# Kernel tuning notes

Hardware: AMD Instinct MI355X
Metric: run time of the kernel (lower is better)

The kernel has to match this reference:

```python
import jax, jax.numpy as jnp
import numpy as np

N, OUT, IN = 16384, 2048, 2048

def setup_inputs() -> dict:
    key = jax.random.key(0)
    k1, k2, k3 = jax.random.split(key, 3)
    input_ = jax.random.normal(k1, (N, IN), dtype=jnp.float32)
    # kaiming normal, fan_in mode: std = sqrt(2/fan_in)
    weight = jax.random.normal(k2, (OUT, IN), dtype=jnp.float32) * np.sqrt(2.0 / IN)
    mask = jax.random.randint(k3, (OUT, IN), 0, 2, dtype=jnp.int32)
    return {"input_": input_, "weight": weight, "mask": mask}

def reference(input_, weight, mask):
    # out = x @ (W * mask)^T  -- mask is a fixed binary expander pattern
    masked_w = weight * mask.astype(weight.dtype)  # [OUT, IN]
    return jnp.matmul(input_, masked_w.T)          # [N, OUT]
```

## Files before the change

### kernel.cpp

```cpp
#include <hip/hip_runtime.h>


#define MDIM 16384
#define NDIM 2048
#define KDIM 2048

#define BM 256
#define BN 256
#define GRID_X ((MDIM / BM) * (NDIM / BN))

using f32x4   = __attribute__((ext_vector_type(4))) float;
using bf16x8  = __attribute__((ext_vector_type(8))) __bf16;
using ushort8 = __attribute__((ext_vector_type(8))) unsigned short;

typedef __attribute__((address_space(3))) const unsigned short* lds_cptr_t;

__device__ __forceinline__ unsigned short f2bf(float f) {
  unsigned int u = __builtin_bit_cast(unsigned int, f);
  u = u + 0x7FFFu + ((u >> 16) & 1u);
  return (unsigned short)(u >> 16);
}


__global__ void convert_input_kernel(const float* __restrict__ in,
                                     unsigned short* __restrict__ out) {
  size_t base = ((size_t)blockIdx.x * blockDim.x + threadIdx.x) * 8;
  float4 a = *reinterpret_cast<const float4*>(in + base);
  float4 b = *reinterpret_cast<const float4*>(in + base + 4);
  ushort8 v;
  v[0] = f2bf(a.x); v[1] = f2bf(a.y); v[2] = f2bf(a.z); v[3] = f2bf(a.w);
  v[4] = f2bf(b.x); v[5] = f2bf(b.y); v[6] = f2bf(b.z); v[7] = f2bf(b.w);
  *reinterpret_cast<ushort8*>(out + base) = v;
}

__global__ void convert_weight_kernel(const float* __restrict__ w,
                                      const int* __restrict__ mk,
                                      unsigned short* __restrict__ out) {
  size_t base = ((size_t)blockIdx.x * blockDim.x + threadIdx.x) * 8;
  float4 a = *reinterpret_cast<const float4*>(w + base);
  float4 b = *reinterpret_cast<const float4*>(w + base + 4);
  int4 m0 = *reinterpret_cast<const int4*>(mk + base);
  int4 m1 = *reinterpret_cast<const int4*>(mk + base + 4);
  ushort8 v;
  v[0] = m0.x ? f2bf(a.x) : (unsigned short)0;
  v[1] = m0.y ? f2bf(a.y) : (unsigned short)0;
  v[2] = m0.z ? f2bf(a.z) : (unsigned short)0;
  v[3] = m0.w ? f2bf(a.w) : (unsigned short)0;
  v[4] = m1.x ? f2bf(b.x) : (unsigned short)0;
  v[5] = m1.y ? f2bf(b.y) : (unsigned short)0;
  v[6] = m1.z ? f2bf(b.z) : (unsigned short)0;
  v[7] = m1.w ? f2bf(b.w) : (unsigned short)0;
  *reinterpret_cast<ushort8*>(out + base) = v;
}


__device__ __forceinline__ f32x4 MF(bf16x8 a, bf16x8 b, f32x4 c) {
  return __builtin_amdgcn_mfma_f32_16x16x32_bf16(a, b, c, 0, 0, 0);
}
#define VMCNT(n) asm volatile("s_waitcnt vmcnt(" #n ")" ::: "memory")
#define DSR(dst, p, off)                                                        \
  asm volatile("ds_read_b128 %0, %1 offset:%2" : "=v"(dst) : "v"(p), "i"(off))

__global__ __launch_bounds__(512, 2) void gemm_asm(
    const unsigned short* __restrict__ Abf,
    const unsigned short* __restrict__ Bbf,
    float* __restrict__ C) {
  __shared__ __attribute__((aligned(16))) unsigned short Asl[4 * 8192];
  __shared__ __attribute__((aligned(16))) unsigned short Bsl[4 * 8192];

  int bid = blockIdx.x;
  int wgs = (bid & 7) * (GRID_X / 8) + (bid >> 3);
  int tm = wgs >> 3;
  int tn = wgs & 7;
  int row0 = tm * BM, col0 = tn * BN;

  int t = threadIdx.x;
  int lane = t & 63, wid = t >> 6;
  int wr = wid >> 2, wc = wid & 3;
  int fr = lane & 15, fq = lane >> 4;

  int p0 = (wid * 2) * 64 + lane;
  int r0 = p0 >> 2, kc0 = ((p0 & 3) ^ ((r0 >> 1) & 3)) * 8;
  size_t offA0 = (size_t)(row0 + r0) * KDIM + kc0;
  size_t offB0 = (size_t)(col0 + r0) * KDIM + kc0;
  int ldsw0 = (wid * 2) * 512;

  int kxor = (fq ^ ((fr >> 1) & 3)) * 8;
  int aoff = (wr * 128 + fr) * 32 + kxor;
  int boff = (wc * 64 + fr) * 32 + kxor;
  lds_cptr_t aA = ((lds_cptr_t)Asl) + aoff;
  lds_cptr_t aB = ((lds_cptr_t)Bsl) + boff;

  f32x4 acc[8][4];
#pragma unroll
  for (int m = 0; m < 8; ++m)
#pragma unroll
    for (int n = 0; n < 4; ++n) acc[m][n] = f32x4{0.f, 0.f, 0.f, 0.f};

#define SLOT_A(b, kh) (Asl + ((b) * 2 + (kh)) * 8192)
#define SLOT_B(b, kh) (Bsl + ((b) * 2 + (kh)) * 8192)

#define STG(slot, base, o0, ke) do {                                            \
  __builtin_amdgcn_global_load_lds(                                             \
      (const __attribute__((address_space(1))) void*)((base) + (o0) + (ke)),    \
      (__attribute__((address_space(3))) void*)((slot) + ldsw0), 16, 0, 0);     \
  __builtin_amdgcn_global_load_lds(                                             \
      (const __attribute__((address_space(1))) void*)((base) + (o0) + 32768 +   \
                                                      (ke)),                    \
      (__attribute__((address_space(3))) void*)((slot) + ldsw0 + 512), 16, 0,   \
      0);                                                                       \
} while (0)

#define PHASE(b, kh, STAGES, WAITS) do {                                        \
  bf16x8 _afr[8], _bfr[4];                                                      \
  DSR(_afr[0], aA, ((b) * 2 + (kh)) * 16384 + 0 * 1024);                        \
  DSR(_afr[1], aA, ((b) * 2 + (kh)) * 16384 + 1 * 1024);                        \
  DSR(_afr[2], aA, ((b) * 2 + (kh)) * 16384 + 2 * 1024);                        \
  DSR(_afr[3], aA, ((b) * 2 + (kh)) * 16384 + 3 * 1024);                        \
  DSR(_afr[4], aA, ((b) * 2 + (kh)) * 16384 + 4 * 1024);                        \
  DSR(_afr[5], aA, ((b) * 2 + (kh)) * 16384 + 5 * 1024);                        \
  DSR(_afr[6], aA, ((b) * 2 + (kh)) * 16384 + 6 * 1024);                        \
  DSR(_afr[7], aA, ((b) * 2 + (kh)) * 16384 + 7 * 1024);                        \
  DSR(_bfr[0], aB, ((b) * 2 + (kh)) * 16384 + 0 * 1024);                        \
  DSR(_bfr[1], aB, ((b) * 2 + (kh)) * 16384 + 1 * 1024);                        \
  DSR(_bfr[2], aB, ((b) * 2 + (kh)) * 16384 + 2 * 1024);                        \
  DSR(_bfr[3], aB, ((b) * 2 + (kh)) * 16384 + 3 * 1024);                        \
  STAGES;                                                                       \
  WAITS;                                                                        \
  __builtin_amdgcn_s_barrier();                                                 \
  asm volatile("s_waitcnt lgkmcnt(0)" ::: "memory");                            \
  __builtin_amdgcn_sched_barrier(0);                                            \
  __builtin_amdgcn_s_setprio(1);                                                \
  _Pragma("unroll")                                                             \
  for (int _m = 0; _m < 8; ++_m)                                                \
    _Pragma("unroll")                                                           \
    for (int _n = 0; _n < 4; ++_n)                                              \
      acc[_m][_n] = MF(_afr[_m], _bfr[_n], acc[_m][_n]);                        \
  __builtin_amdgcn_s_setprio(0);                                                \
  __builtin_amdgcn_s_barrier();                                                 \
} while (0)

  STG(SLOT_A(0, 0), Abf, offA0, 0);
  STG(SLOT_B(0, 0), Bbf, offB0, 0);
  STG(SLOT_A(0, 1), Abf, offA0, 32);
  STG(SLOT_B(0, 1), Bbf, offB0, 32);
  STG(SLOT_A(1, 0), Abf, offA0, 64);
  STG(SLOT_B(1, 0), Bbf, offB0, 64);
  VMCNT(8);
  __builtin_amdgcn_s_barrier();

  for (int i = 0; i < 15; ++i) {
    int kb = i * 128;
    PHASE(0, 0, { STG(SLOT_A(1, 1), Abf, offA0, kb + 96);
                  STG(SLOT_B(1, 1), Bbf, offB0, kb + 96); }, VMCNT(8));
    PHASE(0, 1, { STG(SLOT_A(0, 0), Abf, offA0, kb + 128);
                  STG(SLOT_B(0, 0), Bbf, offB0, kb + 128); }, VMCNT(8));
    PHASE(1, 0, { STG(SLOT_A(0, 1), Abf, offA0, kb + 160);
                  STG(SLOT_B(0, 1), Bbf, offB0, kb + 160); }, VMCNT(8));
    PHASE(1, 1, { STG(SLOT_A(1, 0), Abf, offA0, kb + 192);
                  STG(SLOT_B(1, 0), Bbf, offB0, kb + 192); }, VMCNT(8));
  }
  {
    int kb = (15) * 128;
    PHASE(0, 0, { STG(SLOT_A(1, 1), Abf, offA0, kb + 96);
                  STG(SLOT_B(1, 1), Bbf, offB0, kb + 96); }, VMCNT(8));
    PHASE(0, 1, , VMCNT(4));
    PHASE(1, 0, , VMCNT(0));
    PHASE(1, 1, , );
  }

  size_t crow = (size_t)(row0 + wr * 128 + fq * 4);
  int ccol = col0 + wc * 64 + fr;
#pragma unroll
  for (int m = 0; m < 8; ++m)
#pragma unroll
    for (int n = 0; n < 4; ++n) {
      float* cp = C + (crow + m * 16) * NDIM + ccol + n * 16;
#pragma unroll
      for (int e = 0; e < 4; ++e) cp[(size_t)e * NDIM] = acc[m][n][e];
    }
#undef PHASE
#undef STG
#undef SLOT_A
#undef SLOT_B
}


__global__ __launch_bounds__(256) void gemm_fused_fallback(
    const float* __restrict__ Afp,
    const float* __restrict__ Wfp,
    const int* __restrict__ Mk,
    float* __restrict__ C) {
  __shared__ unsigned short As[128 * 32];
  __shared__ unsigned short Bs[128 * 32];
  int bid = blockIdx.x;
  int nwg = (MDIM / 128) * (NDIM / 128);
  int wg = (bid & 7) * (nwg / 8) + (bid >> 3);
  int tm = wg >> 4, tn = wg & 15;
  int row0 = tm * 128, col0 = tn * 128;
  int t = threadIdx.x;
  int lane = t & 63, wv = t >> 6;
  int wr = wv >> 1, wc = wv & 1;
  int fr = lane & 15, fq = lane >> 4;
  f32x4 acc[4][4];
#pragma unroll
  for (int i = 0; i < 4; ++i)
#pragma unroll
    for (int j = 0; j < 4; ++j) acc[i][j] = f32x4{0.f, 0.f, 0.f, 0.f};
  for (int kt = 0; kt < KDIM; kt += 32) {
#pragma unroll
    for (int j = 0; j < 2; ++j) {
      int c = j * 256 + t;
      int r = c >> 2;
      int ko = (c & 3) * 8;
      const float* ga = Afp + (size_t)(row0 + r) * KDIM + kt + ko;
      float4 a0 = *reinterpret_cast<const float4*>(ga);
      float4 a1 = *reinterpret_cast<const float4*>(ga + 4);
      ushort8 va;
      va[0] = f2bf(a0.x); va[1] = f2bf(a0.y); va[2] = f2bf(a0.z); va[3] = f2bf(a0.w);
      va[4] = f2bf(a1.x); va[5] = f2bf(a1.y); va[6] = f2bf(a1.z); va[7] = f2bf(a1.w);
      *reinterpret_cast<ushort8*>(As + (size_t)c * 8) = va;
      const float* gw = Wfp + (size_t)(col0 + r) * KDIM + kt + ko;
      const int* gm = Mk + (size_t)(col0 + r) * KDIM + kt + ko;
      float4 w0 = *reinterpret_cast<const float4*>(gw);
      float4 w1 = *reinterpret_cast<const float4*>(gw + 4);
      int4 m0 = *reinterpret_cast<const int4*>(gm);
      int4 m1 = *reinterpret_cast<const int4*>(gm + 4);
      ushort8 vb;
      vb[0] = m0.x ? f2bf(w0.x) : (unsigned short)0;
      vb[1] = m0.y ? f2bf(w0.y) : (unsigned short)0;
      vb[2] = m0.z ? f2bf(w0.z) : (unsigned short)0;
      vb[3] = m0.w ? f2bf(w0.w) : (unsigned short)0;
      vb[4] = m1.x ? f2bf(w1.x) : (unsigned short)0;
      vb[5] = m1.y ? f2bf(w1.y) : (unsigned short)0;
      vb[6] = m1.z ? f2bf(w1.z) : (unsigned short)0;
      vb[7] = m1.w ? f2bf(w1.w) : (unsigned short)0;
      *reinterpret_cast<ushort8*>(Bs + (size_t)c * 8) = vb;
    }
    __syncthreads();
    bf16x8 af[4], bfr[4];
#pragma unroll
    for (int m2 = 0; m2 < 4; ++m2)
      af[m2] = *reinterpret_cast<const bf16x8*>(As + (wr * 64 + m2 * 16 + fr) * 32 + fq * 8);
#pragma unroll
    for (int n2 = 0; n2 < 4; ++n2)
      bfr[n2] = *reinterpret_cast<const bf16x8*>(Bs + (wc * 64 + n2 * 16 + fr) * 32 + fq * 8);
#pragma unroll
    for (int m2 = 0; m2 < 4; ++m2)
#pragma unroll
      for (int n2 = 0; n2 < 4; ++n2)
        acc[m2][n2] = MF(af[m2], bfr[n2], acc[m2][n2]);
    __syncthreads();
  }
#pragma unroll
  for (int m2 = 0; m2 < 4; ++m2)
#pragma unroll
    for (int n2 = 0; n2 < 4; ++n2) {
      size_t r0 = (size_t)(row0 + wr * 64 + m2 * 16 + fq * 4);
      size_t c0 = (size_t)(col0 + wc * 64 + n2 * 16 + fr);
#pragma unroll
      for (int i = 0; i < 4; ++i) C[(r0 + i) * NDIM + c0] = acc[m2][n2][i];
    }
}


extern "C" void kernel_launch(void* const* d_in, const int* in_sizes, int n_in,
                              void* d_out, int out_size, void* d_ws, size_t ws_size,
                              hipStream_t stream) {
  const float* input  = (const float*)d_in[0];
  const float* weight = (const float*)d_in[1];
  const int*   mask   = (const int*)d_in[2];
  float* out = (float*)d_out;

  const size_t needA = (size_t)MDIM * KDIM * sizeof(unsigned short);
  const size_t needB = (size_t)NDIM * KDIM * sizeof(unsigned short);

  if (ws_size >= needA + needB) {
    unsigned short* Abf = (unsigned short*)d_ws;
    unsigned short* Bbf = (unsigned short*)((char*)d_ws + needA);
    convert_input_kernel<<<(MDIM * (size_t)KDIM / 8) / 256, 256, 0, stream>>>(input, Abf);
    convert_weight_kernel<<<(NDIM * (size_t)KDIM / 8) / 256, 256, 0, stream>>>(weight, mask, Bbf);
    gemm_asm<<<GRID_X, 512, 0, stream>>>(Abf, Bbf, out);
  } else {
    int nwg = (MDIM / 128) * (NDIM / 128);
    gemm_fused_fallback<<<nwg, 256, 0, stream>>>(input, weight, mask, out);
  }
}
```

Measured before the change: 174.6 us.

## Double-buffer LDS fragment reads in registers across GEMM phases

Measured after the change: 173.1 us. Within noise of the previous version (-0.9%).

```diff
diff --git a/kernel.cpp b/kernel.cpp
--- a/kernel.cpp
+++ b/kernel.cpp
@@ -61,7 +61,7 @@
 #define DSR(dst, p, off)                                                        \
   asm volatile("ds_read_b128 %0, %1 offset:%2" : "=v"(dst) : "v"(p), "i"(off))
 
-__global__ __launch_bounds__(512, 2) void gemm_asm(
+__global__ __launch_bounds__(512, 2) void gemm_ra(
     const unsigned short* __restrict__ Abf,
     const unsigned short* __restrict__ Bbf,
     float* __restrict__ C) {
@@ -96,6 +96,8 @@
   for (int m = 0; m < 8; ++m)
 #pragma unroll
     for (int n = 0; n < 4; ++n) acc[m][n] = f32x4{0.f, 0.f, 0.f, 0.f};
+
+  bf16x8 aP[8], bP[4], aQ[8], bQ[4];
 
 #define SLOT_A(b, kh) (Asl + ((b) * 2 + (kh)) * 8192)
 #define SLOT_B(b, kh) (Bsl + ((b) * 2 + (kh)) * 8192)
@@ -111,20 +113,22 @@
       0);                                                                       \
 } while (0)
 
-#define PHASE(b, kh, STAGES, WAITS) do {                                        \
-  bf16x8 _afr[8], _bfr[4];                                                      \
-  DSR(_afr[0], aA, ((b) * 2 + (kh)) * 16384 + 0 * 1024);                        \
-  DSR(_afr[1], aA, ((b) * 2 + (kh)) * 16384 + 1 * 1024);                        \
-  DSR(_afr[2], aA, ((b) * 2 + (kh)) * 16384 + 2 * 1024);                        \
-  DSR(_afr[3], aA, ((b) * 2 + (kh)) * 16384 + 3 * 1024);                        \
-  DSR(_afr[4], aA, ((b) * 2 + (kh)) * 16384 + 4 * 1024);                        \
-  DSR(_afr[5], aA, ((b) * 2 + (kh)) * 16384 + 5 * 1024);                        \
-  DSR(_afr[6], aA, ((b) * 2 + (kh)) * 16384 + 6 * 1024);                        \
-  DSR(_afr[7], aA, ((b) * 2 + (kh)) * 16384 + 7 * 1024);                        \
-  DSR(_bfr[0], aB, ((b) * 2 + (kh)) * 16384 + 0 * 1024);                        \
-  DSR(_bfr[1], aB, ((b) * 2 + (kh)) * 16384 + 1 * 1024);                        \
-  DSR(_bfr[2], aB, ((b) * 2 + (kh)) * 16384 + 2 * 1024);                        \
-  DSR(_bfr[3], aB, ((b) * 2 + (kh)) * 16384 + 3 * 1024);                        \
+#define RD12(b, kh, AD, BD) do {                                                \
+  DSR(AD[0], aA, ((b) * 2 + (kh)) * 16384 + 0 * 1024);                          \
+  DSR(AD[1], aA, ((b) * 2 + (kh)) * 16384 + 1 * 1024);                          \
+  DSR(AD[2], aA, ((b) * 2 + (kh)) * 16384 + 2 * 1024);                          \
+  DSR(AD[3], aA, ((b) * 2 + (kh)) * 16384 + 3 * 1024);                          \
+  DSR(AD[4], aA, ((b) * 2 + (kh)) * 16384 + 4 * 1024);                          \
+  DSR(AD[5], aA, ((b) * 2 + (kh)) * 16384 + 5 * 1024);                          \
+  DSR(AD[6], aA, ((b) * 2 + (kh)) * 16384 + 6 * 1024);                          \
+  DSR(AD[7], aA, ((b) * 2 + (kh)) * 16384 + 7 * 1024);                          \
+  DSR(BD[0], aB, ((b) * 2 + (kh)) * 16384 + 0 * 1024);                          \
+  DSR(BD[1], aB, ((b) * 2 + (kh)) * 16384 + 1 * 1024);                          \
+  DSR(BD[2], aB, ((b) * 2 + (kh)) * 16384 + 2 * 1024);                          \
+  DSR(BD[3], aB, ((b) * 2 + (kh)) * 16384 + 3 * 1024);                          \
+} while (0)
+
+#define PHASE(rb, rkh, AC, BC, AD, BD, STAGES, WAITS) do {                      \
   STAGES;                                                                       \
   WAITS;                                                                        \
   __builtin_amdgcn_s_barrier();                                                 \
@@ -132,10 +136,16 @@
   __builtin_amdgcn_sched_barrier(0);                                            \
   __builtin_amdgcn_s_setprio(1);                                                \
   _Pragma("unroll")                                                             \
-  for (int _m = 0; _m < 8; ++_m)                                                \
+  for (int _m = 0; _m < 4; ++_m)                                                \
     _Pragma("unroll")                                                           \
     for (int _n = 0; _n < 4; ++_n)                                              \
-      acc[_m][_n] = MF(_afr[_m], _bfr[_n], acc[_m][_n]);                        \
+      acc[_m][_n] = MF(AC[_m], BC[_n], acc[_m][_n]);                            \
+  RD12(rb, rkh, AD, BD);                                                        \
+  _Pragma("unroll")                                                             \
+  for (int _m = 4; _m < 8; ++_m)                                                \
+    _Pragma("unroll")                                                           \
+    for (int _n = 0; _n < 4; ++_n)                                              \
+      acc[_m][_n] = MF(AC[_m], BC[_n], acc[_m][_n]);                            \
   __builtin_amdgcn_s_setprio(0);                                                \
   __builtin_amdgcn_s_barrier();                                                 \
 } while (0)
@@ -148,25 +158,36 @@
   STG(SLOT_B(1, 0), Bbf, offB0, 64);
   VMCNT(8);
   __builtin_amdgcn_s_barrier();
+  RD12(0, 0, aP, bP);
 
   for (int i = 0; i < 15; ++i) {
     int kb = i * 128;
-    PHASE(0, 0, { STG(SLOT_A(1, 1), Abf, offA0, kb + 96);
-                  STG(SLOT_B(1, 1), Bbf, offB0, kb + 96); }, VMCNT(8));
-    PHASE(0, 1, { STG(SLOT_A(0, 0), Abf, offA0, kb + 128);
-                  STG(SLOT_B(0, 0), Bbf, offB0, kb + 128); }, VMCNT(8));
-    PHASE(1, 0, { STG(SLOT_A(0, 1), Abf, offA0, kb + 160);
-                  STG(SLOT_B(0, 1), Bbf, offB0, kb + 160); }, VMCNT(8));
-    PHASE(1, 1, { STG(SLOT_A(1, 0), Abf, offA0, kb + 192);
-                  STG(SLOT_B(1, 0), Bbf, offB0, kb + 192); }, VMCNT(8));
+    PHASE(0, 1, aP, bP, aQ, bQ, { STG(SLOT_A(1, 1), Abf, offA0, kb + 96);
+                                  STG(SLOT_B(1, 1), Bbf, offB0, kb + 96); },
+          VMCNT(8));
+    PHASE(1, 0, aQ, bQ, aP, bP, { STG(SLOT_A(0, 0), Abf, offA0, kb + 128);
+                                  STG(SLOT_B(0, 0), Bbf, offB0, kb + 128); },
+          VMCNT(8));
+    PHASE(1, 1, aP, bP, aQ, bQ, { STG(SLOT_A(0, 1), Abf, offA0, kb + 160);
+                                  STG(SLOT_B(0, 1), Bbf, offB0, kb + 160); },
+          VMCNT(8));
+    PHASE(0, 0, aQ, bQ, aP, bP, { STG(SLOT_A(1, 0), Abf, offA0, kb + 192);
+                                  STG(SLOT_B(1, 0), Bbf, offB0, kb + 192); },
+          VMCNT(8));
   }
+  PHASE(0, 1, aP, bP, aQ, bQ, { STG(SLOT_A(1, 1), Abf, offA0, 2016);
+                                STG(SLOT_B(1, 1), Bbf, offB0, 2016); },
+        VMCNT(8));
+  PHASE(1, 0, aQ, bQ, aP, bP, , VMCNT(4));
+  PHASE(1, 1, aP, bP, aQ, bQ, , VMCNT(0));
   {
-    int kb = (15) * 128;
-    PHASE(0, 0, { STG(SLOT_A(1, 1), Abf, offA0, kb + 96);
-                  STG(SLOT_B(1, 1), Bbf, offB0, kb + 96); }, VMCNT(8));
-    PHASE(0, 1, , VMCNT(4));
-    PHASE(1, 0, , VMCNT(0));
-    PHASE(1, 1, , );
+    asm volatile("s_waitcnt lgkmcnt(0)" ::: "memory");
+    __builtin_amdgcn_sched_barrier(0);
+#pragma unroll
+    for (int m = 0; m < 8; ++m)
+#pragma unroll
+      for (int n = 0; n < 4; ++n)
+        acc[m][n] = MF(aQ[m], bQ[n], acc[m][n]);
   }
 
   size_t crow = (size_t)(row0 + wr * 128 + fq * 4);
@@ -180,6 +201,7 @@
       for (int e = 0; e < 4; ++e) cp[(size_t)e * NDIM] = acc[m][n][e];
     }
 #undef PHASE
+#undef RD12
 #undef STG
 #undef SLOT_A
 #undef SLOT_B
@@ -280,7 +302,7 @@
     unsigned short* Bbf = (unsigned short*)((char*)d_ws + needA);
     convert_input_kernel<<<(MDIM * (size_t)KDIM / 8) / 256, 256, 0, stream>>>(input, Abf);
     convert_weight_kernel<<<(NDIM * (size_t)KDIM / 8) / 256, 256, 0, stream>>>(weight, mask, Bbf);
-    gemm_asm<<<GRID_X, 512, 0, stream>>>(Abf, Bbf, out);
+    gemm_ra<<<GRID_X, 512, 0, stream>>>(Abf, Bbf, out);
   } else {
     int nwg = (MDIM / 128) * (NDIM / 128);
     gemm_fused_fallback<<<nwg, 256, 0, stream>>>(input, weight, mask, out);
```
